# Kernel optimization log

Hardware: AMD Instinct MI355X
Metric: run time of the kernel (lower is better)

The kernel has to match this reference:

```python
import jax, jax.numpy as jnp
import numpy as np

N, IN, OUT, RANK = 8192, 4096, 4096, 256

def setup_inputs() -> dict:
    key = jax.random.key(0)
    ks = jax.random.split(key, 7)
    x = jax.random.normal(ks[0], (N, IN), dtype=jnp.float32)
    # original frozen linear layer params
    W = jax.random.normal(ks[1], (OUT, IN), dtype=jnp.float32) * (1.0 / np.sqrt(IN))
    bias = jax.random.normal(ks[2], (OUT,), dtype=jnp.float32) * 0.01
    # frozen shared low-rank matrices (kaiming-uniform-like scale)
    A_frozen = jax.random.normal(ks[3], (RANK, IN), dtype=jnp.float32) * (1.0 / np.sqrt(IN))
    B_frozen = jax.random.normal(ks[4], (OUT, RANK), dtype=jnp.float32) * (1.0 / np.sqrt(RANK))
    # trainable VeRA vectors (b_vec is zeros at init; use small randn so delta is nonzero)
    b_vec = jax.random.normal(ks[5], (OUT,), dtype=jnp.float32) * 0.01
    d_vec = jnp.full((RANK,), 0.1, dtype=jnp.float32) + jax.random.normal(ks[6], (RANK,), dtype=jnp.float32) * 0.01
    return {"x": x, "W": W, "bias": bias, "A_frozen": A_frozen, "B_frozen": B_frozen, "b_vec": b_vec, "d_vec": d_vec}

def reference(x, W, bias, A_frozen, B_frozen, b_vec, d_vec):
    # original frozen linear: [N, OUT]
    orig = x @ W.T + bias
    # diag(b) @ B @ diag(d) @ A @ x.T  ==  (((x @ A.T) * d) @ B.T) * b, transposed
    h = (x @ A_frozen.T) * d_vec            # [N, RANK]
    delta = (h @ B_frozen.T) * b_vec        # [N, OUT]
    return orig + delta
```

## Files before the change

### kernel.cpp

```cpp
#include <hip/hip_runtime.h>

#define IN_DIM 4096
#define OUT_DIM 4096
#define N_ROWS 8192
#define RANK 256

typedef __bf16 bf16x8 __attribute__((ext_vector_type(8)));
typedef float f32x4 __attribute__((ext_vector_type(4)));
typedef unsigned short u16;
typedef unsigned short u16x4 __attribute__((ext_vector_type(4)));

__device__ __forceinline__ u16 f2b(float f) {
    unsigned int u = __builtin_bit_cast(unsigned int, f);
    unsigned int r = u + 0x7FFFu + ((u >> 16) & 1u);
    return (u16)(r >> 16);
}

__device__ __forceinline__ void async16(const void* g, const void* l) {
    __builtin_amdgcn_global_load_lds(
        (const __attribute__((address_space(1))) void*)g,
        (__attribute__((address_space(3))) void*)l, 16, 0, 0);
}

__global__ __launch_bounds__(256) void cvt4(const float* __restrict__ s,
                                            u16* __restrict__ d, int n4) {
    int i = blockIdx.x * 256 + threadIdx.x;
    if (i >= n4) return;
    f32x4 v = __builtin_nontemporal_load((const f32x4*)s + i);
    u16x4 o;
    o.x = f2b(v.x); o.y = f2b(v.y); o.z = f2b(v.z); o.w = f2b(v.w);
    *((u16x4*)d + i) = o;
}

__global__ __launch_bounds__(256) void vera_adt(const float* __restrict__ A,
                                                const float* __restrict__ d,
                                                u16* __restrict__ adt) {
    int r = threadIdx.x;
    int i0 = blockIdx.x * 64;
    float dv = d[r];
    const float* ap = A + (size_t)r * IN_DIM + i0;
#pragma unroll 4
    for (int j = 0; j < 64; ++j)
        adt[(size_t)(i0 + j) * RANK + r] = f2b(__builtin_nontemporal_load(ap + j) * dv);
}

template <int MODE, int K, int NN, int TM, int TN>
__global__ __launch_bounds__(256) void vera_gemm(
    const u16* __restrict__ Aop, const u16* __restrict__ Bop,
    const float* __restrict__ W, const float* __restrict__ bvec,
    void* __restrict__ outv) {
    __shared__ __align__(16) __bf16 As[128 * 32];
    __shared__ __align__(16) __bf16 Bs[128 * 32];

    const int tid = threadIdx.x;
    const int lane = tid & 63;
    const int wavei = __builtin_amdgcn_readfirstlane(tid >> 6);
    const int fr = lane & 15;
    const int fq = lane >> 4;
    const int wm = (wavei >> 1) * 64;
    const int wn = (wavei & 1) * 64;

    constexpr int G = 8;
    const int bid = blockIdx.x;
    const int g = bid / (G * TN);
    const int r = bid - g * (G * TN);
    const int bm = (g * G + (r & (G - 1))) * 128;
    const int bn = (r / G) * 128;

    const int srow = tid >> 2;
    const int sk = (tid & 3) * 8;
    const u16* ga0 = Aop + (size_t)(bm + srow) * K + sk;
    const u16* ga1 = Aop + (size_t)(bm + 64 + srow) * K + sk;
    const u16* gb0 = Bop + (size_t)(bn + srow) * K + sk;
    const u16* gb1 = Bop + (size_t)(bn + 64 + srow) * K + sk;

    char* lAs = (char*)As;
    char* lBs = (char*)Bs;
    const int lo = wavei * 1024;

    f32x4 acc[4][4] = {};

    for (int k0 = 0; k0 < K; k0 += 32) {
        __syncthreads();
        async16(ga0 + k0, lAs + lo);
        async16(ga1 + k0, lAs + 4096 + lo);
        async16(gb0 + k0, lBs + lo);
        async16(gb1 + k0, lBs + 4096 + lo);
        __syncthreads();

        const __bf16* ap = As + (wm + fr) * 32 + fq * 8;
        const __bf16* bp = Bs + (wn + fr) * 32 + fq * 8;
        bf16x8 af[4], bfr[4];
#pragma unroll
        for (int i = 0; i < 4; ++i) {
            af[i] = *(const bf16x8*)(ap + i * 16 * 32);
            bfr[i] = *(const bf16x8*)(bp + i * 16 * 32);
        }
#pragma unroll
        for (int mi = 0; mi < 4; ++mi)
#pragma unroll
            for (int ni = 0; ni < 4; ++ni)
                acc[mi][ni] = __builtin_amdgcn_mfma_f32_16x16x32_bf16(
                    af[mi], bfr[ni], acc[mi][ni], 0, 0, 0);
    }

#pragma unroll
    for (int ni = 0; ni < 4; ++ni) {
        const int col = bn + wn + ni * 16 + fr;
        float bcol = (MODE == 1) ? bvec[col] : 0.f;
#pragma unroll
        for (int mi = 0; mi < 4; ++mi) {
            const int row0 = bm + wm + mi * 16 + fq * 4;
#pragma unroll
            for (int v = 0; v < 4; ++v) {
                const int row = row0 + v;
                float a = acc[mi][ni][v];
                if (MODE == 0) {
                    float wv = __builtin_nontemporal_load(&W[(size_t)row * NN + col]);
                    ((u16*)outv)[(size_t)row * NN + col] = f2b(wv + bvec[row] * a);
                } else {
                    __builtin_nontemporal_store(a + bcol,
                        &((float*)outv)[(size_t)row * NN + col]);
                }
            }
        }
    }
}

extern "C" void kernel_launch(void* const* d_in, const int* in_sizes, int n_in,
                              void* d_out, int out_size, void* d_ws, size_t ws_size,
                              hipStream_t stream) {
    (void)in_sizes; (void)n_in; (void)out_size; (void)ws_size;
    const float* x    = (const float*)d_in[0];
    const float* W    = (const float*)d_in[1];
    const float* bias = (const float*)d_in[2];
    const float* A    = (const float*)d_in[3];
    const float* B    = (const float*)d_in[4];
    const float* bv   = (const float*)d_in[5];
    const float* dv   = (const float*)d_in[6];

    char* ws = (char*)d_ws;
    u16* xb  = (u16*)ws;
    u16* wb  = (u16*)(ws + (size_t)N_ROWS * IN_DIM * 2);
    u16* adt = (u16*)(ws + (size_t)N_ROWS * IN_DIM * 2
                         + (size_t)OUT_DIM * IN_DIM * 2);
    u16* Bb  = adt + (size_t)IN_DIM * RANK;

    cvt4<<<dim3(OUT_DIM * RANK / 4 / 256), 256, 0, stream>>>(B, Bb, OUT_DIM * RANK / 4);
    vera_adt<<<dim3(IN_DIM / 64), 256, 0, stream>>>(A, dv, adt);
    vera_gemm<0, RANK, IN_DIM, OUT_DIM / 128, IN_DIM / 128>
        <<<dim3((OUT_DIM / 128) * (IN_DIM / 128)), 256, 0, stream>>>(
        Bb, adt, W, bv, wb);
    cvt4<<<dim3(N_ROWS * IN_DIM / 4 / 256), 256, 0, stream>>>(x, xb, N_ROWS * IN_DIM / 4);
    vera_gemm<1, IN_DIM, OUT_DIM, N_ROWS / 128, OUT_DIM / 128>
        <<<dim3((N_ROWS / 128) * (OUT_DIM / 128)), 256, 0, stream>>>(
        xb, wb, nullptr, bias, d_out);
}
```

Baseline: 612.5 us.

## Replace main GEMM with 256x256-tile, 8-wave, multi-stage pipelined kernel

Swaps the main x@W' GEMM for a new kernel that uses 256x256 output tiles and 512 threads. It stages K in four 16KB LDS slots using async global-to-LDS loads with partial vmcnt waits, XOR-swizzles the LDS layout against bank conflicts, and raises MFMA priority with setprio. The aim is to hide global load latency behind MFMA work and improve operand reuse over the old single-buffered 128x128 kernel, which had two barriers per 32-wide K step. In exchange it uses 128KB of LDS and a large accumulator register footprint, which limits occupancy, and the hand-written waitcnt/barrier schedule is fragile.

Result: faster. 542.2 us (-11.5%).

```diff
diff --git a/kernel.cpp b/kernel.cpp
--- a/kernel.cpp
+++ b/kernel.cpp
@@ -127,6 +127,127 @@
     }
 }
 
+#define BARW() do { __builtin_amdgcn_s_barrier(); \
+    asm volatile("s_waitcnt lgkmcnt(0)" ::: "memory"); \
+    __builtin_amdgcn_sched_barrier(0); } while (0)
+#define W6()   asm volatile("s_waitcnt vmcnt(6)" ::: "memory")
+#define ENDP() __builtin_amdgcn_s_barrier()
+
+template <int K, int MT, int NTL>
+__global__ __launch_bounds__(512, 2) void gemm256(
+    const u16* __restrict__ Aop, const u16* __restrict__ Bop,
+    const float* __restrict__ bvec, float* __restrict__ out) {
+    constexpr int NTK = K / 64;
+    __shared__ __align__(16) char lds[131072];
+    char* const L = (char*)lds;
+
+    const int tid = threadIdx.x;
+    const int lane = tid & 63;
+    const int wavei = __builtin_amdgcn_readfirstlane(tid >> 6);
+    const int fr = lane & 15;
+    const int fq = lane >> 4;
+    const int wmi = wavei >> 2;
+    const int wni = wavei & 3;
+
+    constexpr int NWG = MT * NTL;
+    const int bid = blockIdx.x;
+    const int idx = (bid & 7) * (NWG / 8) + (bid >> 3);
+    const int bm = (idx % MT) * 256;
+    const int bn = (idx / MT) * 256;
+
+    const int c0 = wavei * 128 + lane;
+    const int r0 = c0 >> 2;
+    const int k0of = ((c0 & 3) ^ ((r0 >> 1) & 3)) * 8;
+    const int c1 = c0 + 64;
+    const int r1 = c1 >> 2;
+    const int k1of = ((c1 & 3) ^ ((r1 >> 1) & 3)) * 8;
+    const u16* gA0 = Aop + (size_t)(bm + r0) * K + k0of;
+    const u16* gA1 = Aop + (size_t)(bm + r1) * K + k1of;
+    const u16* gB0 = Bop + (size_t)(bn + r0) * K + k0of;
+    const u16* gB1 = Bop + (size_t)(bn + r1) * K + k1of;
+    const int wl = wavei * 2048;
+
+    auto stageA = [&](int tau, int j, int slot) {
+        const int kb = tau * 64 + j * 32;
+        async16(gA0 + kb, L + slot * 16384 + wl);
+        async16(gA1 + kb, L + slot * 16384 + wl + 1024);
+    };
+    auto stageB = [&](int tau, int j, int slot) {
+        const int kb = tau * 64 + j * 32;
+        async16(gB0 + kb, L + 65536 + slot * 16384 + wl);
+        async16(gB1 + kb, L + 65536 + slot * 16384 + wl + 1024);
+    };
+
+    const int aswz = ((fq ^ ((fr >> 1) & 3)) << 4);
+    const int aoff = (wmi * 128 + fr) * 64 + aswz;
+    const int boff = 65536 + (wni * 64 + fr) * 64 + aswz;
+
+    bf16x8 af[4], bf[4];
+    f32x4 acc[8][4] = {};
+
+    auto ldA = [&](int slot, int mh) {
+        const char* p = L + slot * 16384 + aoff + mh * 4096;
+#pragma unroll
+        for (int i = 0; i < 4; ++i) af[i] = *(const bf16x8*)(p + i * 1024);
+    };
+    auto ldB = [&](int slot) {
+        const char* p = L + slot * 16384 + boff;
+#pragma unroll
+        for (int i = 0; i < 4; ++i) bf[i] = *(const bf16x8*)(p + i * 1024);
+    };
+    auto MF = [&](int mh) {
+        __builtin_amdgcn_s_setprio(1);
+#pragma unroll
+        for (int mi = 0; mi < 4; ++mi)
+#pragma unroll
+            for (int ni = 0; ni < 4; ++ni)
+                acc[mh * 4 + mi][ni] = __builtin_amdgcn_mfma_f32_16x16x32_bf16(
+                    af[mi], bf[ni], acc[mh * 4 + mi][ni], 0, 0, 0);
+        __builtin_amdgcn_s_setprio(0);
+    };
+
+    stageA(0, 0, 0); stageB(0, 0, 0);
+    stageA(0, 1, 1); stageB(0, 1, 1);
+    stageA(1, 0, 2);
+    asm volatile("s_waitcnt vmcnt(6)" ::: "memory");
+    __builtin_amdgcn_s_barrier();
+
+#pragma unroll 1
+    for (int it = 0; it < NTK / 2; ++it) {
+        const int t  = 2 * it;
+        const int t1 = t + 1;
+        const int t2 = (t + 2 < NTK) ? t + 2 : NTK - 1;
+        const int t3 = (t + 3 < NTK) ? t + 3 : NTK - 1;
+
+        ldA(0, 0); ldB(0); stageB(t1, 0, 2); BARW(); MF(0); ENDP();
+        ldA(0, 1);         stageA(t1, 1, 3); BARW(); MF(1); W6(); ENDP();
+        ldA(1, 0); ldB(1); stageB(t1, 1, 3); BARW(); MF(0); ENDP();
+        ldA(1, 1);         stageA(t2, 0, 0); BARW(); MF(1); W6(); ENDP();
+        ldA(2, 0); ldB(2); stageB(t2, 0, 0); BARW(); MF(0); ENDP();
+        ldA(2, 1);         stageA(t2, 1, 1); BARW(); MF(1); W6(); ENDP();
+        ldA(3, 0); ldB(3); stageB(t2, 1, 1); BARW(); MF(0); ENDP();
+        ldA(3, 1);         stageA(t3, 0, 2); BARW(); MF(1); W6(); ENDP();
+    }
+
+    asm volatile("s_waitcnt vmcnt(0)" ::: "memory");
+
+    const int colb = bn + wni * 64 + fr;
+    const int rowb = bm + wmi * 128 + fq * 4;
+#pragma unroll
+    for (int ni = 0; ni < 4; ++ni) {
+        const int col = colb + ni * 16;
+        const float bc = bvec[col];
+#pragma unroll
+        for (int m8 = 0; m8 < 8; ++m8) {
+            const int row = rowb + (m8 >> 2) * 64 + (m8 & 3) * 16;
+#pragma unroll
+            for (int v = 0; v < 4; ++v)
+                __builtin_nontemporal_store(acc[m8][ni][v] + bc,
+                    &out[(size_t)(row + v) * (NTL * 256) + col]);
+        }
+    }
+}
+
 extern "C" void kernel_launch(void* const* d_in, const int* in_sizes, int n_in,
                               void* d_out, int out_size, void* d_ws, size_t ws_size,
                               hipStream_t stream) {
@@ -152,7 +273,7 @@
         <<<dim3((OUT_DIM / 128) * (IN_DIM / 128)), 256, 0, stream>>>(
         Bb, adt, W, bv, wb);
     cvt4<<<dim3(N_ROWS * IN_DIM / 4 / 256), 256, 0, stream>>>(x, xb, N_ROWS * IN_DIM / 4);
-    vera_gemm<1, IN_DIM, OUT_DIM, N_ROWS / 128, OUT_DIM / 128>
-        <<<dim3((N_ROWS / 128) * (OUT_DIM / 128)), 256, 0, stream>>>(
-        xb, wb, nullptr, bias, d_out);
-}
+    gemm256<IN_DIM, N_ROWS / 256, OUT_DIM / 256>
+        <<<dim3((N_ROWS / 256) * (OUT_DIM / 256)), 512, 0, stream>>>(
+        xb, wb, bias, (float*)d_out);
+}
```
